# Kernel tuning notes

Measured on AMD Instinct MI355X. Metric: run time of the kernel, lower is better.

## Reference

```python
import jax, jax.numpy as jnp
import numpy as np

EMBED_DIM = 1024
NUM_HEADS = 16
HEAD_DIM = EMBED_DIM // NUM_HEADS


def setup_inputs() -> dict:
    key = jax.random.key(0)
    ks = jax.random.split(key, 11)
    B, T, D = 4, 2048, EMBED_DIM
    s = 1.0 / np.sqrt(D)
    inp = {
        "x": jax.random.normal(ks[0], (B, T, D), dtype=jnp.float32),
        "wq": jax.random.normal(ks[1], (D, D), dtype=jnp.float32) * s,
        "bq": jnp.zeros((D,), dtype=jnp.float32),
        "wk": jax.random.normal(ks[2], (D, D), dtype=jnp.float32) * s,
        "bk": jnp.zeros((D,), dtype=jnp.float32),
        "wv": jax.random.normal(ks[3], (D, D), dtype=jnp.float32) * s,
        "bv": jnp.zeros((D,), dtype=jnp.float32),
        "wo": jax.random.normal(ks[4], (D, D), dtype=jnp.float32) * s,
        "bo": jnp.zeros((D,), dtype=jnp.float32),
        "ln_gamma": jnp.ones((D,), dtype=jnp.float32),
        "ln_beta": jnp.zeros((D,), dtype=jnp.float32),
    }
    return inp


def _attention(x, wq, bq, wk, bk, wv, bv, wo, bo, ln_gamma, ln_beta):
    B, T, D = x.shape
    H, Hd = NUM_HEADS, HEAD_DIM
    # projections -> (B, H, T, Hd)
    q = (x @ wq + bq).reshape(B, T, H, Hd).transpose(0, 2, 1, 3)
    k = (x @ wk + bk).reshape(B, T, H, Hd).transpose(0, 2, 1, 3)
    v = (x @ wv + bv).reshape(B, T, H, Hd).transpose(0, 2, 1, 3)
    scores = jnp.einsum("bhqd,bhkd->bhqk", q, k) / jnp.sqrt(jnp.asarray(Hd, x.dtype))
    attn = jax.nn.softmax(scores, axis=-1)  # dropout p=0 -> identity
    out = jnp.einsum("bhqk,bhkd->bhqd", attn, v)
    out = out.transpose(0, 2, 1, 3).reshape(B, T, D)
    out = out @ wo + bo
    # LayerNorm (no residual in the original forward)
    mu = jnp.mean(out, axis=-1, keepdims=True)
    var = jnp.var(out, axis=-1, keepdims=True)
    out = (out - mu) / jnp.sqrt(var + 1e-5) * ln_gamma + ln_beta
    return out


def reference(x, wq, bq, wk, bk, wv, bv, wo, bo, ln_gamma, ln_beta):
    return _attention(x, wq, bq, wk, bk, wv, bv, wo, bo, ln_gamma, ln_beta)
```

## Files before the change

kernel.cpp:

```cpp
#include <hip/hip_runtime.h>
#include <hip/hip_bf16.h>

typedef __bf16 bf16_t;
typedef __bf16 bf16x4v __attribute__((ext_vector_type(4)));
typedef __bf16 bf16x8 __attribute__((ext_vector_type(8)));
typedef float  f32x4  __attribute__((ext_vector_type(4)));

typedef __attribute__((address_space(1))) void* gptr_t;
typedef __attribute__((address_space(3))) void* lptr_t;

#define B_BATCH  4
#define T_SEQ    2048
#define D_MODEL  1024
#define N_HEADS  16
#define HEAD_DIM 64
#define M_ROWS   (B_BATCH * T_SEQ)

#define BM  128
#define BN  128
#define BKK 64
#define LDT 72
#define CPAD 136

#define EXP2_SCALE 0.1803368801111204f

__global__ __launch_bounds__(256) void cvt_x(
    const float* __restrict__ in, bf16_t* __restrict__ out)
{
    const size_t i = ((size_t)blockIdx.x * 256 + threadIdx.x) * 4;
    const f32x4 v = *(const f32x4*)&in[i];
    bf16x4v o;
    for (int e = 0; e < 4; e++) o[e] = (bf16_t)v[e];
    *(bf16x4v*)&out[i] = o;
}

__global__ __launch_bounds__(256) void transpose_w(
    const float* __restrict__ w0, const float* __restrict__ w1,
    const float* __restrict__ w2, const float* __restrict__ w3,
    bf16_t* __restrict__ out)
{
    __shared__ bf16_t tile[32][33];
    const int z = blockIdx.z;
    const float* w = (z == 0) ? w0 : (z == 1) ? w1 : (z == 2) ? w2 : w3;
    bf16_t* o = out + (size_t)z * D_MODEL * D_MODEL;
    const int tx = threadIdx.x & 31, ty = threadIdx.x >> 5;
    const int k0 = blockIdx.y * 32, n0 = blockIdx.x * 32;
    for (int i = 0; i < 4; i++)
        tile[ty + i * 8][tx] = (bf16_t)w[(size_t)(k0 + ty + i * 8) * D_MODEL + n0 + tx];
    __syncthreads();
    for (int i = 0; i < 4; i++)
        o[(size_t)(n0 + ty + i * 8) * D_MODEL + k0 + tx] = tile[tx][ty + i * 8];
}

template <int MODE>
__global__ __launch_bounds__(256) void gemm_k(
    const bf16_t* __restrict__ A, const bf16_t* __restrict__ wT_base,
    const float* __restrict__ b0, const float* __restrict__ b1,
    void* __restrict__ out_base)
{
    __shared__ __attribute__((aligned(16))) bf16_t smem[17408];
    bf16_t (*As)[BKK]  = reinterpret_cast<bf16_t(*)[BKK]>(&smem[0]);
    bf16_t (*Bs)[BKK]  = reinterpret_cast<bf16_t(*)[BKK]>(&smem[8192]);
    bf16_t (*Cs)[CPAD] = reinterpret_cast<bf16_t(*)[CPAD]>(&smem[0]);

    const int tid  = threadIdx.x;
    const int z    = blockIdx.z;
    const bf16_t* BT   = wT_base + (size_t)z * D_MODEL * D_MODEL;
    const float*  bias = (z == 0) ? b0 : b1;
    const int mbase = blockIdx.y * BM;
    const int nbase = blockIdx.x * BN;
    const int w = tid >> 6, lane = tid & 63, quad = lane >> 4, l16 = lane & 15;
    const int wm = (w & 1) * 64, wn = (w >> 1) * 64;
    const int lrow = lane >> 3, lcol = (lane & 7) * 8;

    f32x4 acc[4][4] = {};

    for (int kb = 0; kb < D_MODEL; kb += BKK) {
        __syncthreads();
        for (int it = 0; it < 4; it++) {
            const int r = w * 32 + it * 8;
            __builtin_amdgcn_global_load_lds(
                (gptr_t)&A [(size_t)(mbase + r + lrow) * D_MODEL + kb + lcol],
                (lptr_t)&As[r][0], 16, 0, 0);
            __builtin_amdgcn_global_load_lds(
                (gptr_t)&BT[(size_t)(nbase + r + lrow) * D_MODEL + kb + lcol],
                (lptr_t)&Bs[r][0], 16, 0, 0);
        }
        __syncthreads();
        for (int s = 0; s < 2; s++) {
            bf16x8 af[4], bf[4];
            for (int i = 0; i < 4; i++)
                af[i] = *(const bf16x8*)&As[wm + i * 16 + l16][s * 32 + quad * 8];
            for (int j = 0; j < 4; j++)
                bf[j] = *(const bf16x8*)&Bs[wn + j * 16 + l16][s * 32 + quad * 8];
            for (int i = 0; i < 4; i++)
                for (int j = 0; j < 4; j++)
                    acc[i][j] = __builtin_amdgcn_mfma_f32_16x16x32_bf16(
                        af[i], bf[j], acc[i][j], 0, 0, 0);
        }
    }

    float bj[4];
    for (int j = 0; j < 4; j++)
        bj[j] = bias[nbase + wn + j * 16 + l16];

    if (MODE == 1) {
        for (int i = 0; i < 4; i++)
            for (int r = 0; r < 4; r++) {
                const int rg = mbase + wm + i * 16 + quad * 4 + r;
                for (int j = 0; j < 4; j++) {
                    const int cg = nbase + wn + j * 16 + l16;
                    ((float*)out_base)[(size_t)rg * D_MODEL + cg] = acc[i][j][r] + bj[j];
                }
            }
    } else {
        __syncthreads();
        for (int i = 0; i < 4; i++)
            for (int r = 0; r < 4; r++) {
                const int row = wm + i * 16 + quad * 4 + r;
                for (int j = 0; j < 4; j++) {
                    const int col = wn + j * 16 + l16;
                    const float v = acc[i][j][r] + bj[j];
                    if (MODE == 0) Cs[row][col] = (bf16_t)v;
                    else           Cs[col][row] = (bf16_t)v;
                }
            }
        __syncthreads();

        const int bidx  = mbase >> 11;
        const int t0    = mbase & 2047;
        const int hbase = nbase >> 6;
        bf16_t* outp = (bf16_t*)out_base;
        for (int p = 0; p < 8; p++) {
            const int chunk = p * 256 + tid;
            if (MODE == 0) {
                const int sub = chunk & 7, run = chunk >> 3;
                const int t = run & 127, hl = run >> 7;
                const bf16x8 val = *(const bf16x8*)&Cs[t][hl * 64 + sub * 8];
                bf16_t* q = outp + (size_t)z * ((size_t)M_ROWS * D_MODEL);
                *(bf16x8*)&q[(((size_t)(bidx * N_HEADS + hbase + hl)) * T_SEQ + t0 + t)
                             * HEAD_DIM + sub * 8] = val;
            } else {
                const int sub = chunk & 15, hdl = chunk >> 4;
                const int h = hbase + (hdl >> 6), hd = hdl & 63;
                const bf16x8 val = *(const bf16x8*)&Cs[hdl][sub * 8];
                *(bf16x8*)&outp[(((size_t)(bidx * N_HEADS + h)) * HEAD_DIM + hd) * T_SEQ
                                + t0 + sub * 8] = val;
            }
        }
    }
}

__global__ __launch_bounds__(256, 4) void attn_k(
    const bf16_t* __restrict__ Q, const bf16_t* __restrict__ K,
    const bf16_t* __restrict__ VT, bf16_t* __restrict__ O)
{
    __shared__ __attribute__((aligned(16))) bf16_t Ks[64][LDT];
    __shared__ __attribute__((aligned(16))) bf16_t Vs[64][LDT];
    __shared__ __attribute__((aligned(16))) bf16_t Ps[4][32][LDT];

    const int tid = threadIdx.x;
    const int f = blockIdx.y * 16 + blockIdx.x;
    const int xcd = f & 7, j = f >> 3;
    const int bh = xcd * 8 + (j & 7);
    const int qbase = (j >> 3) * 128;
    const int b = bh >> 4, h = bh & 15;
    const int w = tid >> 6, lane = tid & 63, quad = lane >> 4, l16 = lane & 15;
    const size_t head_off = (size_t)bh * T_SEQ * HEAD_DIM;
    const bf16_t* Qh  = Q  + head_off;
    const bf16_t* Kh  = K  + head_off;
    const bf16_t* VTh = VT + head_off;

    bf16x8 bq[2][2];
    for (int iq = 0; iq < 2; iq++)
        for (int s = 0; s < 2; s++)
            bq[iq][s] = *(const bf16x8*)
                &Qh[(size_t)(qbase + w * 32 + iq * 16 + l16) * HEAD_DIM + s * 32 + quad * 8];

    float l_part[2] = {0.f, 0.f};
    f32x4 Oacc[2][4] = {};

    for (int kt = 0; kt < T_SEQ / 64; kt++) {
        const int kbase = kt * 64;
        __syncthreads();
        for (int it = 0; it < 2; it++) {
            int idx = it * 256 + tid;
            int r = idx >> 3, c8 = (idx & 7) * 8;
            *(bf16x8*)&Ks[r][c8] = *(const bf16x8*)&Kh [(size_t)(kbase + r) * HEAD_DIM + c8];
            *(bf16x8*)&Vs[r][c8] = *(const bf16x8*)&VTh[(size_t)r * T_SEQ + kbase + c8];
        }
        __syncthreads();

        f32x4 St[4][2] = {};
        for (int s = 0; s < 2; s++) {
            bf16x8 ak[4];
            for (int jk = 0; jk < 4; jk++)
                ak[jk] = *(const bf16x8*)&Ks[jk * 16 + l16][s * 32 + quad * 8];
            for (int jk = 0; jk < 4; jk++)
                for (int iq = 0; iq < 2; iq++)
                    St[jk][iq] = __builtin_amdgcn_mfma_f32_16x16x32_bf16(
                        ak[jk], bq[iq][s], St[jk][iq], 0, 0, 0);
        }

        for (int jk = 0; jk < 4; jk++)
            for (int iq = 0; iq < 2; iq++) {
                bf16x4v pv;
                for (int r = 0; r < 4; r++) {
                    const float p = __builtin_amdgcn_exp2f(St[jk][iq][r] * EXP2_SCALE);
                    l_part[iq] += p;
                    pv[r] = (bf16_t)p;
                }
                *(bf16x4v*)&Ps[w][iq * 16 + l16][jk * 16 + quad * 4] = pv;
            }
        asm volatile("" ::: "memory");

        for (int s = 0; s < 2; s++) {
            bf16x8 ap[2], bv[4];
            for (int iq = 0; iq < 2; iq++)
                ap[iq] = *(const bf16x8*)&Ps[w][iq * 16 + l16][s * 32 + quad * 8];
            for (int jn = 0; jn < 4; jn++)
                bv[jn] = *(const bf16x8*)&Vs[jn * 16 + l16][s * 32 + quad * 8];
            for (int iq = 0; iq < 2; iq++)
                for (int jn = 0; jn < 4; jn++)
                    Oacc[iq][jn] = __builtin_amdgcn_mfma_f32_16x16x32_bf16(
                        ap[iq], bv[jn], Oacc[iq][jn], 0, 0, 0);
        }
    }

    for (int iq = 0; iq < 2; iq++) {
        l_part[iq] += __shfl_xor(l_part[iq], 16, 64);
        l_part[iq] += __shfl_xor(l_part[iq], 32, 64);
    }

    for (int iq = 0; iq < 2; iq++) {
        for (int r = 0; r < 4; r++) {
            const int qrow = quad * 4 + r;
            const float inv = 1.f / __shfl(l_part[iq], qrow, 64);
            const int t = qbase + w * 32 + iq * 16 + qrow;
            for (int jn = 0; jn < 4; jn++) {
                const int hd = jn * 16 + l16;
                O[(((size_t)(b * T_SEQ + t)) * N_HEADS + h) * HEAD_DIM + hd] =
                    (bf16_t)(Oacc[iq][jn][r] * inv);
            }
        }
    }
}

__global__ __launch_bounds__(256) void ln_k(
    const float* __restrict__ proj, const float* __restrict__ gamma,
    const float* __restrict__ beta, float* __restrict__ out)
{
    __shared__ float red[4][2];
    const int row = blockIdx.x, tid = threadIdx.x;
    const float* p = proj + (size_t)row * D_MODEL + tid * 4;
    const f32x4 v = *(const f32x4*)p;
    float s1 = v[0] + v[1] + v[2] + v[3];
    float s2 = v[0] * v[0] + v[1] * v[1] + v[2] * v[2] + v[3] * v[3];
    for (int off = 32; off >= 1; off >>= 1) {
        s1 += __shfl_xor(s1, off, 64);
        s2 += __shfl_xor(s2, off, 64);
    }
    const int w = tid >> 6;
    if ((tid & 63) == 0) { red[w][0] = s1; red[w][1] = s2; }
    __syncthreads();
    const float S1 = red[0][0] + red[1][0] + red[2][0] + red[3][0];
    const float S2 = red[0][1] + red[1][1] + red[2][1] + red[3][1];
    const float mu  = S1 * (1.f / D_MODEL);
    const float var = S2 * (1.f / D_MODEL) - mu * mu;
    const float rstd = rsqrtf(var + 1e-5f);
    const int c = tid * 4;
    f32x4 o;
    for (int e = 0; e < 4; e++)
        o[e] = (v[e] - mu) * rstd * gamma[c + e] + beta[c + e];
    *(f32x4*)&out[(size_t)row * D_MODEL + c] = o;
}

extern "C" void kernel_launch(void* const* d_in, const int* in_sizes, int n_in,
                              void* d_out, int out_size, void* d_ws, size_t ws_size,
                              hipStream_t stream)
{
    const float* x  = (const float*)d_in[0];
    const float* wq = (const float*)d_in[1];
    const float* bq = (const float*)d_in[2];
    const float* wk = (const float*)d_in[3];
    const float* bk = (const float*)d_in[4];
    const float* wv = (const float*)d_in[5];
    const float* bv = (const float*)d_in[6];
    const float* wo = (const float*)d_in[7];
    const float* bo = (const float*)d_in[8];
    const float* g  = (const float*)d_in[9];
    const float* be = (const float*)d_in[10];

    char* ws = (char*)d_ws;
    bf16_t* xb   = (bf16_t*)(ws);
    bf16_t* wT   = (bf16_t*)(ws + ((size_t)16 << 20));
    bf16_t* qkv  = (bf16_t*)(ws + ((size_t)24 << 20));
    bf16_t* attn = (bf16_t*)(ws + ((size_t)72 << 20));
    float*  proj = (float*) (ws + ((size_t)88 << 20));
    bf16_t* vt   = (bf16_t*)proj;

    cvt_x<<<dim3(M_ROWS * D_MODEL / 1024), 256, 0, stream>>>(x, xb);
    transpose_w<<<dim3(32, 32, 4), 256, 0, stream>>>(wq, wk, wv, wo, wT);

    gemm_k<0><<<dim3(8, 64, 2), 256, 0, stream>>>(xb, wT, bq, bk, (void*)qkv);
    gemm_k<2><<<dim3(8, 64, 1), 256, 0, stream>>>(
        xb, wT + (size_t)2 * D_MODEL * D_MODEL, bv, bv, (void*)vt);

    bf16_t* Qm = qkv;
    bf16_t* Km = qkv + (size_t)M_ROWS * D_MODEL;

    attn_k<<<dim3(16, 64), 256, 0, stream>>>(Qm, Km, vt, attn);

    gemm_k<1><<<dim3(8, 64, 1), 256, 0, stream>>>(
        attn, wT + (size_t)3 * D_MODEL * D_MODEL, bo, bo, (void*)proj);

    ln_k<<<dim3(M_ROWS), 256, 0, stream>>>(proj, g, be, (float*)d_out);
}
```

Baseline: 317.2 us.

## Double-buffer attention K/V tiles with direct global-to-LDS loads and XOR swizzle

The attention kernel now stages K and V^T tiles through two LDS buffers. Each tile is filled with global_load_lds, which writes straight into shared memory, and the load for the next tile is issued before the current tile is computed, so memory latency can overlap the MFMA work. The padded LDS rows are replaced by unpadded 64-wide rows with an XOR swizzle on 16-byte chunks to avoid bank conflicts. MFMA bursts are wrapped in s_setprio to favour the matrix work. The risk is correctness: the code relies on the barrier waiting for the asynchronous LDS DMA to land before the buffer is read.

Result: slower. 339.3 us (+7.0%).

```diff
diff --git a/kernel.cpp b/kernel.cpp
--- a/kernel.cpp
+++ b/kernel.cpp
@@ -155,8 +155,8 @@
     const bf16_t* __restrict__ Q, const bf16_t* __restrict__ K,
     const bf16_t* __restrict__ VT, bf16_t* __restrict__ O)
 {
-    __shared__ __attribute__((aligned(16))) bf16_t Ks[64][LDT];
-    __shared__ __attribute__((aligned(16))) bf16_t Vs[64][LDT];
+    __shared__ __attribute__((aligned(16))) bf16_t Ks[2][64 * 64];
+    __shared__ __attribute__((aligned(16))) bf16_t Vs[2][64 * 64];
     __shared__ __attribute__((aligned(16))) bf16_t Ps[4][32][LDT];
 
     const int tid = threadIdx.x;
@@ -171,35 +171,64 @@
     const bf16_t* Kh  = K  + head_off;
     const bf16_t* VTh = VT + head_off;
 
+    const int srow = lane >> 3;
+    const int scol = ((lane & 7) ^ srow) * 8;
+
+    const int rxor = l16 & 7;
+    const int rc0 = ((0 + quad) ^ rxor) * 8;
+    const int rc1 = ((4 + quad) ^ rxor) * 8;
+
     bf16x8 bq[2][2];
     for (int iq = 0; iq < 2; iq++)
         for (int s = 0; s < 2; s++)
             bq[iq][s] = *(const bf16x8*)
                 &Qh[(size_t)(qbase + w * 32 + iq * 16 + l16) * HEAD_DIM + s * 32 + quad * 8];
 
+    for (int it = 0; it < 2; it++) {
+        const int R = w * 16 + it * 8;
+        __builtin_amdgcn_global_load_lds(
+            (gptr_t)&Kh[(size_t)(R + srow) * HEAD_DIM + scol],
+            (lptr_t)&Ks[0][R * 64], 16, 0, 0);
+        __builtin_amdgcn_global_load_lds(
+            (gptr_t)&VTh[(size_t)(R + srow) * T_SEQ + scol],
+            (lptr_t)&Vs[0][R * 64], 16, 0, 0);
+    }
+
     float l_part[2] = {0.f, 0.f};
     f32x4 Oacc[2][4] = {};
 
     for (int kt = 0; kt < T_SEQ / 64; kt++) {
-        const int kbase = kt * 64;
-        __syncthreads();
-        for (int it = 0; it < 2; it++) {
-            int idx = it * 256 + tid;
-            int r = idx >> 3, c8 = (idx & 7) * 8;
-            *(bf16x8*)&Ks[r][c8] = *(const bf16x8*)&Kh [(size_t)(kbase + r) * HEAD_DIM + c8];
-            *(bf16x8*)&Vs[r][c8] = *(const bf16x8*)&VTh[(size_t)r * T_SEQ + kbase + c8];
-        }
-        __syncthreads();
+        __syncthreads();
+        const bf16_t* Kc = Ks[kt & 1];
+        const bf16_t* Vc = Vs[kt & 1];
+
+        if (kt + 1 < T_SEQ / 64) {
+            const int kb2 = (kt + 1) * 64;
+            bf16_t* Kn = Ks[(kt + 1) & 1];
+            bf16_t* Vn = Vs[(kt + 1) & 1];
+            for (int it = 0; it < 2; it++) {
+                const int R = w * 16 + it * 8;
+                __builtin_amdgcn_global_load_lds(
+                    (gptr_t)&Kh[(size_t)(kb2 + R + srow) * HEAD_DIM + scol],
+                    (lptr_t)&Kn[R * 64], 16, 0, 0);
+                __builtin_amdgcn_global_load_lds(
+                    (gptr_t)&VTh[(size_t)(R + srow) * T_SEQ + kb2 + scol],
+                    (lptr_t)&Vn[R * 64], 16, 0, 0);
+            }
+        }
 
         f32x4 St[4][2] = {};
         for (int s = 0; s < 2; s++) {
+            const int rc = s ? rc1 : rc0;
             bf16x8 ak[4];
             for (int jk = 0; jk < 4; jk++)
-                ak[jk] = *(const bf16x8*)&Ks[jk * 16 + l16][s * 32 + quad * 8];
+                ak[jk] = *(const bf16x8*)&Kc[(jk * 16 + l16) * 64 + rc];
+            __builtin_amdgcn_s_setprio(1);
             for (int jk = 0; jk < 4; jk++)
                 for (int iq = 0; iq < 2; iq++)
                     St[jk][iq] = __builtin_amdgcn_mfma_f32_16x16x32_bf16(
                         ak[jk], bq[iq][s], St[jk][iq], 0, 0, 0);
+            __builtin_amdgcn_s_setprio(0);
         }
 
         for (int jk = 0; jk < 4; jk++)
@@ -215,15 +244,18 @@
         asm volatile("" ::: "memory");
 
         for (int s = 0; s < 2; s++) {
+            const int rc = s ? rc1 : rc0;
             bf16x8 ap[2], bv[4];
             for (int iq = 0; iq < 2; iq++)
                 ap[iq] = *(const bf16x8*)&Ps[w][iq * 16 + l16][s * 32 + quad * 8];
             for (int jn = 0; jn < 4; jn++)
-                bv[jn] = *(const bf16x8*)&Vs[jn * 16 + l16][s * 32 + quad * 8];
+                bv[jn] = *(const bf16x8*)&Vc[(jn * 16 + l16) * 64 + rc];
+            __builtin_amdgcn_s_setprio(1);
             for (int iq = 0; iq < 2; iq++)
                 for (int jn = 0; jn < 4; jn++)
                     Oacc[iq][jn] = __builtin_amdgcn_mfma_f32_16x16x32_bf16(
                         ap[iq], bv[jn], Oacc[iq][jn], 0, 0, 0);
+            __builtin_amdgcn_s_setprio(0);
         }
     }
 
```
